# Optimization experiments

Hardware: AMD Instinct MI355X
Metric: run time of the kernel (lower is better)

## Reference

```python
import jax, jax.numpy as jnp
import numpy as np

B, N, E, H, KVC = 2, 1024, 512, 8, 1536  # KVC = 3*E, head_dim = E//H = 64
EPS = 1e-5  # torch InstanceNorm2d default eps


def instance_norm(x):
    # normalize over the last two (spatial) dims per (batch, channel); biased var, no affine
    mu = jnp.mean(x, axis=(-2, -1), keepdims=True)
    var = jnp.var(x, axis=(-2, -1), keepdims=True)
    return (x - mu) * jax.lax.rsqrt(var + EPS)


def _heads(x):
    # [B, T, E] -> [B, H, T, E//H]
    b, t, e = x.shape
    return x.reshape(b, t, H, e // H).transpose(0, 2, 1, 3)


def setup_inputs() -> dict:
    key = jax.random.key(0)
    ks = jax.random.split(key, 16)
    s_e = 1.0 / np.sqrt(E)
    s_c = 1.0 / np.sqrt(KVC)
    inp = {
        'emb1': jax.random.normal(ks[0], (B, N, E), jnp.float32),
        'emb2': jax.random.normal(ks[1], (B, N, E), jnp.float32),
        'emb3': jax.random.normal(ks[2], (B, N, E), jnp.float32),
        'emb_C': jax.random.normal(ks[3], (B, N, KVC), jnp.float32),
        'Wq1': jax.random.normal(ks[4], (E, E), jnp.float32) * s_e,
        'Wq2': jax.random.normal(ks[5], (E, E), jnp.float32) * s_e,
        'Wq3': jax.random.normal(ks[6], (E, E), jnp.float32) * s_e,
        'Wk': jax.random.normal(ks[7], (E, E), jnp.float32) * s_e,
        'Wv': jax.random.normal(ks[8], (E, E), jnp.float32) * s_e,
        'WqC': jax.random.normal(ks[9], (KVC, KVC), jnp.float32) * s_c,
        'WkC': jax.random.normal(ks[10], (KVC, KVC), jnp.float32) * s_c,
        'WvC': jax.random.normal(ks[11], (KVC, KVC), jnp.float32) * s_c,
        'Wo1': jax.random.normal(ks[12], (E, E), jnp.float32) * s_e,
        'Wo2': jax.random.normal(ks[13], (E, E), jnp.float32) * s_e,
        'Wo3': jax.random.normal(ks[14], (E, E), jnp.float32) * s_e,
    }
    return inp


def reference(emb1, emb2, emb3, emb_C, Wq1, Wq2, Wq3, Wk, Wv, WqC, WkC, WvC, Wo1, Wo2, Wo3):
    # ---- channel attention over emb_C ----
    Q_C = emb_C @ WqC.T  # [B, N, KVC]
    K_C = emb_C @ WkC.T
    V_C = emb_C @ WvC.T
    attn_c = jnp.einsum('bnc,bnd->bcd', Q_C, K_C)          # [B, KVC, KVC]
    ch_sim = jax.nn.softmax(instance_norm(attn_c), axis=-1)  # psi1 (1 channel) + softmax(dim=3)
    ctx_c = jnp.einsum('bcd,bnd->bcn', ch_sim, V_C)        # [B, KVC, N]
    T_hat = ctx_c.transpose(0, 2, 1)                        # [B, N, KVC]
    # split last dim into 3 chunks of E, concat along token dim -> shared K/V source [B, 3N, E]
    KV_S = jnp.concatenate(jnp.split(T_hat, 3, axis=2), axis=1)

    # ---- spatial attention: 3 query streams share one K/V ----
    K = _heads(KV_S @ Wk.T)                # [B, H, 3N, d]
    V = _heads(KV_S @ Wv.T)                # [B, H, 3N, d]
    Kt = K.transpose(0, 1, 3, 2)           # [B, H, d, 3N]

    def stream(emb, Wq, Wo):
        Q = _heads(emb @ Wq.T)              # [B, H, N, d]
        attn = Q @ Kt                       # [B, H, N, 3N]
        sim = jax.nn.softmax(instance_norm(attn), axis=-1)  # psi2 per (b,h) + softmax
        ctx = sim @ V                       # [B, H, N, d]
        ctx = ctx.transpose(0, 2, 1, 3).reshape(emb.shape[0], emb.shape[1], E)
        return ctx @ Wo.T

    O1 = stream(emb1, Wq1, Wo1)
    O2 = stream(emb2, Wq2, Wo2)
    O3 = stream(emb3, Wq3, Wo3)
    return (O1, O2, O3)
```

## Files before the change

### kernel.cpp

```cpp
#include <hip/hip_runtime.h>
#include <math.h>

#define NTOK 1024
#define EDIM 512
#define KVCH 1536
#define TKV  3072
#define VSTRIDE 6144

typedef __bf16 bf16x8 __attribute__((ext_vector_type(8)));
typedef float f32x4 __attribute__((ext_vector_type(4)));
#define MFMA16(a,b,c) __builtin_amdgcn_mfma_f32_16x16x32_bf16(a,b,c,0,0,0)

__device__ __forceinline__ ushort f2bf(float f){
    uint u = __float_as_uint(f);
    u += 0x7FFFu + ((u>>16)&1u);
    return (ushort)(u>>16);
}
__device__ __forceinline__ float bf2f(ushort h){ return __uint_as_float(((uint)h)<<16); }
__device__ __forceinline__ bf16x8 ldsb8(const ushort* p){ return *(const bf16x8*)p; }

__device__ __forceinline__ void async16(const ushort* g, ushort* l){
    __builtin_amdgcn_global_load_lds((const __attribute__((address_space(1))) void*)g,
                                     (__attribute__((address_space(3))) void*)l, 16, 0, 0);
}

#define NCVT 15
struct CvtJobs { const float* src[NCVT]; ushort* hi[NCVT]; ushort* lo[NCVT]; int n[NCVT]; };

__global__ __launch_bounds__(256) void cvt_hilo(CvtJobs J)
{
    int a = blockIdx.y;
    int i = (blockIdx.x*256 + threadIdx.x)*4;
    if (i >= J.n[a]) return;
    float4 v = *(const float4*)(J.src[a] + i);
    ushort4 h, l;
    h.x=f2bf(v.x); l.x=f2bf(v.x-bf2f(h.x));
    h.y=f2bf(v.y); l.y=f2bf(v.y-bf2f(h.y));
    h.z=f2bf(v.z); l.z=f2bf(v.z-bf2f(h.z));
    h.w=f2bf(v.w); l.w=f2bf(v.w-bf2f(h.w));
    *(ushort4*)(J.hi[a]+i) = h;
    *(ushort4*)(J.lo[a]+i) = l;
}

struct GemmDesc {
    const ushort *Ahi, *Alo, *Bhi, *Blo;
    float* Cf; ushort *Chi, *Clo, *Cthi, *Ctlo;
    double* stats;
    int K, lda, ldb, ldc, ldct;
    int zmod;
    long sA0, sA1, sB0, sB1, sC0, sC1;
};

__global__ __launch_bounds__(256) void mgemmF(GemmDesc D0, GemmDesc D1,
                                              int nblk0, int nx0, int ny0, int nx1, int ny1)
{
    __shared__ ushort Ah[4096], Al[4096], Bh[4096], Bl[4096];
    __shared__ double sred[8];
    const int tid = threadIdx.x;
    int bid = blockIdx.x;
    GemmDesc d; int nx, ny, rel;
    if (bid < nblk0) { d = D0; rel = bid; nx = nx0; ny = ny0; }
    else             { d = D1; rel = bid - nblk0; nx = nx1; ny = ny1; }
    const int bx = rel % nx; int tt = rel / nx;
    const int by = tt % ny;  const int z = tt / ny;
    const int zb = z / d.zmod, zj = z - zb*d.zmod;
    const size_t aoff = (size_t)zb*d.sA0 + (size_t)zj*d.sA1;
    const size_t boff = (size_t)zb*d.sB0 + (size_t)zj*d.sB1;
    const size_t coff = (size_t)zb*d.sC0 + (size_t)zj*d.sC1;
    const int mb = by<<7, nb = bx<<7;
    const int wave = tid>>6, lane = tid&63;
    const int wr = wave>>1, wc = wave&1;
    const int fr = lane&15, fq = lane>>4;
    const int srow = (wave<<5) + (lane>>2);
    const int scg  = (lane&3)<<3;
    f32x4 acc[4][4];
    #pragma unroll
    for (int i=0;i<4;++i)
        #pragma unroll
        for (int j=0;j<4;++j) acc[i][j] = (f32x4){0.f,0.f,0.f,0.f};

    for (int k0=0; k0<d.K; k0+=32) {
        #pragma unroll
        for (int it=0; it<2; ++it) {
            int row = srow + (it<<4);
            int lb = ((wave<<5) + (it<<4)) << 5;
            size_t ga = aoff + (size_t)(mb+row)*d.lda + k0 + scg;
            size_t gb = boff + (size_t)(nb+row)*d.ldb + k0 + scg;
            async16(d.Ahi+ga, &Ah[lb]);
            async16(d.Alo+ga, &Al[lb]);
            async16(d.Bhi+gb, &Bh[lb]);
            async16(d.Blo+gb, &Bl[lb]);
        }
        __syncthreads();
        bf16x8 fah[4], fal[4];
        #pragma unroll
        for (int m=0;m<4;++m) {
            int o = ((wr*64 + m*16 + fr)<<5) + (fq<<3);
            fah[m] = ldsb8(&Ah[o]); fal[m] = ldsb8(&Al[o]);
        }
        #pragma unroll
        for (int n=0;n<4;++n) {
            int o = ((wc*64 + n*16 + fr)<<5) + (fq<<3);
            bf16x8 fbh = ldsb8(&Bh[o]), fbl = ldsb8(&Bl[o]);
            #pragma unroll
            for (int m=0;m<4;++m) {
                acc[m][n] = MFMA16(fah[m], fbh, acc[m][n]);
                acc[m][n] = MFMA16(fah[m], fbl, acc[m][n]);
                acc[m][n] = MFMA16(fal[m], fbh, acc[m][n]);
            }
        }
        __syncthreads();
    }
    #pragma unroll
    for (int m=0;m<4;++m) {
        #pragma unroll
        for (int n=0;n<4;++n) {
            int row = mb + wr*64 + m*16 + fq*4;
            int col = nb + wc*64 + n*16 + fr;
            f32x4 v = acc[m][n];
            if (d.Cf) {
                #pragma unroll
                for (int r=0;r<4;++r) d.Cf[coff + (size_t)(row+r)*d.ldc + col] = v[r];
            }
            if (d.Chi) {
                #pragma unroll
                for (int r=0;r<4;++r) {
                    ushort hh = f2bf(v[r]);
                    size_t o = coff + (size_t)(row+r)*d.ldc + col;
                    d.Chi[o] = hh; d.Clo[o] = f2bf(v[r]-bf2f(hh));
                }
            }
            if (d.Cthi) {
                ushort4 h4, l4;
                #pragma unroll
                for (int r=0;r<4;++r) {
                    ushort hh = f2bf(v[r]);
                    ((ushort*)&h4)[r] = hh;
                    ((ushort*)&l4)[r] = f2bf(v[r]-bf2f(hh));
                }
                size_t o = coff + (size_t)col*d.ldct + row;
                *(ushort4*)(d.Cthi+o) = h4;
                *(ushort4*)(d.Ctlo+o) = l4;
            }
        }
    }
    if (d.stats) {
        double s=0.0, s2=0.0;
        #pragma unroll
        for (int m=0;m<4;++m)
            #pragma unroll
            for (int n=0;n<4;++n)
                #pragma unroll
                for (int r=0;r<4;++r) { double v = acc[m][n][r]; s += v; s2 += v*v; }
        #pragma unroll
        for (int off=32; off; off>>=1) { s += __shfl_xor(s, off); s2 += __shfl_xor(s2, off); }
        if (lane==0){ sred[wave]=s; sred[4+wave]=s2; }
        __syncthreads();
        if (tid==0) {
            atomicAdd(&d.stats[2*zb],   sred[0]+sred[1]+sred[2]+sred[3]);
            atomicAdd(&d.stats[2*zb+1], sred[4]+sred[5]+sred[6]+sred[7]);
        }
    }
}

__global__ __launch_bounds__(256) void chan_softmax(const float* __restrict__ ATT, const double* __restrict__ ST,
                                                    ushort* __restrict__ Shi, ushort* __restrict__ Slo)
{
    int b = blockIdx.y;
    size_t ro = (size_t)b * KVCH * KVCH + (size_t)blockIdx.x * KVCH;
    const float* p = ATT + ro;
    ushort* ph = Shi + ro;
    ushort* pl = Slo + ro;
    double cnt = (double)KVCH * (double)KVCH;
    double mean = ST[2*b] / cnt;
    double var  = ST[2*b+1] / cnt - mean * mean;
    float sc = (float)(1.0 / sqrt(var + 1e-5));
    int tid = threadIdx.x;
    float x[6];
    #pragma unroll
    for (int k = 0; k < 6; ++k) x[k] = p[tid + (k << 8)] * sc;
    float mx = fmaxf(fmaxf(fmaxf(x[0],x[1]),fmaxf(x[2],x[3])),fmaxf(x[4],x[5]));
    #pragma unroll
    for (int m = 32; m; m >>= 1) mx = fmaxf(mx, __shfl_xor(mx, m));
    __shared__ float red[4];
    int w = tid >> 6;
    if ((tid & 63) == 0) red[w] = mx;
    __syncthreads();
    mx = fmaxf(fmaxf(red[0],red[1]), fmaxf(red[2],red[3]));
    __syncthreads();
    float e[6]; float sum = 0.f;
    #pragma unroll
    for (int k = 0; k < 6; ++k) { e[k] = __expf(x[k] - mx); sum += e[k]; }
    #pragma unroll
    for (int m = 32; m; m >>= 1) sum += __shfl_xor(sum, m);
    if ((tid & 63) == 0) red[w] = sum;
    __syncthreads();
    sum = red[0]+red[1]+red[2]+red[3];
    float inv = 1.0f / sum;
    #pragma unroll
    for (int k = 0; k < 6; ++k) {
        float pv = e[k] * inv;
        ushort hh = f2bf(pv);
        ph[tid + (k << 8)] = hh;
        pl[tid + (k << 8)] = f2bf(pv - bf2f(hh));
    }
}

__global__ __launch_bounds__(256) void gram4(
    const ushort* __restrict__ Kbhi, const ushort* __restrict__ Kblo,
    const ushort* __restrict__ QBhi, const ushort* __restrict__ QBlo,
    float* __restrict__ GK, float* __restrict__ SK,
    float* __restrict__ GQ, float* __restrict__ SQm)
{
    int z = blockIdx.z;
    const ushort *Xh, *Xl; int T; float *G, *CS;
    if (z == 0) { Xh=Kbhi; Xl=Kblo; T=TKV; G=GK; CS=SK; }
    else { Xh=QBhi+(size_t)(z-1)*1048576; Xl=QBlo+(size_t)(z-1)*1048576;
           T=NTOK; G=GQ+(size_t)(z-1)*65536; CS=SQm+(size_t)(z-1)*1024; }
    int bh = blockIdx.x;
    int b = bh >> 3, h = bh & 7;
    const ushort* Xbh = Xh + (size_t)b * T * EDIM + h * 64;
    const ushort* Xbl = Xl + (size_t)b * T * EDIM + h * 64;
    int rows = T / gridDim.y;
    int t0 = blockIdx.y * rows;
    __shared__ float Xs[4][64];
    int tid = threadIdx.x;
    int i0 = (tid >> 4) << 2, j0 = (tid & 15) << 2;
    float acc[4][4] = {};
    float cs = 0.f;
    for (int t = t0; t < t0 + rows; t += 4) {
        __syncthreads();
        int r = tid >> 6, c = tid & 63;
        size_t gidx = (size_t)(t + r) * EDIM + c;
        Xs[r][c] = bf2f(Xbh[gidx]) + bf2f(Xbl[gidx]);
        __syncthreads();
        #pragma unroll
        for (int rr = 0; rr < 4; ++rr) {
            float xi0=Xs[rr][i0], xi1=Xs[rr][i0+1], xi2=Xs[rr][i0+2], xi3=Xs[rr][i0+3];
            float xj0=Xs[rr][j0], xj1=Xs[rr][j0+1], xj2=Xs[rr][j0+2], xj3=Xs[rr][j0+3];
            acc[0][0]=fmaf(xi0,xj0,acc[0][0]); acc[0][1]=fmaf(xi0,xj1,acc[0][1]); acc[0][2]=fmaf(xi0,xj2,acc[0][2]); acc[0][3]=fmaf(xi0,xj3,acc[0][3]);
            acc[1][0]=fmaf(xi1,xj0,acc[1][0]); acc[1][1]=fmaf(xi1,xj1,acc[1][1]); acc[1][2]=fmaf(xi1,xj2,acc[1][2]); acc[1][3]=fmaf(xi1,xj3,acc[1][3]);
            acc[2][0]=fmaf(xi2,xj0,acc[2][0]); acc[2][1]=fmaf(xi2,xj1,acc[2][1]); acc[2][2]=fmaf(xi2,xj2,acc[2][2]); acc[2][3]=fmaf(xi2,xj3,acc[2][3]);
            acc[3][0]=fmaf(xi3,xj0,acc[3][0]); acc[3][1]=fmaf(xi3,xj1,acc[3][1]); acc[3][2]=fmaf(xi3,xj2,acc[3][2]); acc[3][3]=fmaf(xi3,xj3,acc[3][3]);
        }
        if (tid < 64) cs += Xs[0][tid] + Xs[1][tid] + Xs[2][tid] + Xs[3][tid];
    }
    float* Gp = G + (size_t)bh * 4096;
    #pragma unroll
    for (int i = 0; i < 4; ++i)
        #pragma unroll
        for (int j = 0; j < 4; ++j)
            atomicAdd(&Gp[(i0 + i) * 64 + j0 + j], acc[i][j]);
    if (tid < 64) atomicAdd(&CS[bh * 64 + tid], cs);
}

__global__ __launch_bounds__(256) void spatial_scale(
    const float* __restrict__ GQ, const float* __restrict__ GK,
    const float* __restrict__ SQm, const float* __restrict__ SKm, float* __restrict__ SVo)
{
    int st = blockIdx.y, bh = blockIdx.x, tid = threadIdx.x;
    const float* gq = GQ + (size_t)st*65536 + bh*4096;
    const float* gk = GK + bh*4096;
    double e2 = 0.0;
    for (int i = tid; i < 4096; i += 256)
        e2 += (double)gq[i] * (double)gk[i];
    double mm = 0.0;
    if (tid < 64) mm = (double)SQm[(size_t)st*1024 + bh*64 + tid] * (double)SKm[bh*64 + tid];
    #pragma unroll
    for (int m = 32; m; m >>= 1) { e2 += __shfl_xor(e2, m); mm += __shfl_xor(mm, m); }
    __shared__ double se[4], sm[4];
    int w = tid >> 6;
    if ((tid & 63) == 0) { se[w] = e2; sm[w] = mm; }
    __syncthreads();
    if (tid == 0) {
        double cnt = (double)NTOK * (double)TKV;
        double E2 = (se[0]+se[1]+se[2]+se[3]) / cnt;
        double M  = (sm[0]+sm[1]+sm[2]+sm[3]) / cnt;
        double var = E2 - M * M;
        SVo[st*16+bh] = (float)(1.0 / sqrt(var + 1e-5));
    }
}

__global__ __launch_bounds__(256) void flash_mfma(
    const ushort* __restrict__ Qhi, const ushort* __restrict__ Qlo,
    const ushort* __restrict__ Khi, const ushort* __restrict__ Klo,
    const ushort* __restrict__ VThi, const ushort* __restrict__ VTlo,
    const float* __restrict__ SV,
    ushort* __restrict__ Ohi, ushort* __restrict__ Olo)
{
    __shared__ ushort Kh[4096], Kl[4096], Vh[4096], Vl[4096], Ph[4096];
    const int st = blockIdx.z, bh = blockIdx.y, b = bh>>3, h = bh&7;
    const int n0 = blockIdx.x<<6;
    const int tid = threadIdx.x, wave = tid>>6, lane = tid&63;
    const int fr = lane&15, fq = lane>>4;
    const float sc = SV[st*16 + bh];
    const size_t qb = (size_t)st*1048576 + (size_t)(b*1024 + n0)*512 + h*64;
    bf16x8 qfh[2], qfl[2];
    {
        const ushort* qph = Qhi + qb + (size_t)(wave*16 + fr)*512;
        const ushort* qpl = Qlo + qb + (size_t)(wave*16 + fr)*512;
        #pragma unroll
        for (int ks=0; ks<2; ++ks) {
            qfh[ks] = ldsb8(qph + ks*32 + fq*8);
            qfl[ks] = ldsb8(qpl + ks*32 + fq*8);
        }
    }
    f32x4 accO[4]; float lsum[4];
    #pragma unroll
    for (int i=0;i<4;++i){ accO[i]=(f32x4){0.f,0.f,0.f,0.f}; lsum[i]=0.f; }
    const size_t kb = (size_t)(b*TKV)*512 + h*64;
    const size_t vb = (size_t)(h*64)*VSTRIDE + b*TKV;
    for (int t0=0; t0<TKV; t0+=64) {
        #pragma unroll
        for (int it=0; it<2; ++it) {
            int r  = (wave<<4) + (it<<3) + (lane>>3);
            int lb = ((wave<<4) + (it<<3)) << 6;
            int gck = ((lane&7) ^ (r&7)) << 3;
            size_t gk = kb + (size_t)(t0+r)*512 + gck;
            size_t gv = vb + (size_t)r*VSTRIDE + t0 + gck;
            async16(Khi+gk, &Kh[lb]);
            async16(Klo+gk, &Kl[lb]);
            async16(VThi+gv, &Vh[lb]);
            async16(VTlo+gv, &Vl[lb]);
        }
        __syncthreads();
        f32x4 s[4];
        #pragma unroll
        for (int i=0;i<4;++i) s[i]=(f32x4){0.f,0.f,0.f,0.f};
        #pragma unroll
        for (int ks=0; ks<2; ++ks) {
            #pragma unroll
            for (int nf=0; nf<4; ++nf) {
                int r = nf*16+fr;
                int ko = (r<<6) + ((ks*32 + fq*8) ^ ((r&7)<<3));
                bf16x8 kh = ldsb8(&Kh[ko]), kl = ldsb8(&Kl[ko]);
                s[nf] = MFMA16(qfh[ks], kh, s[nf]);
                s[nf] = MFMA16(qfh[ks], kl, s[nf]);
                s[nf] = MFMA16(qfl[ks], kh, s[nf]);
            }
        }
        #pragma unroll
        for (int reg=0; reg<4; ++reg) {
            int prow = fq*4+reg;
            float psum = 0.f;
            #pragma unroll
            for (int nf=0;nf<4;++nf){
                float p = __expf(sc * s[nf][reg]);
                psum += p;
                int pidx = (wave<<10) + (prow<<6) + ((nf*16+fr) ^ ((prow&7)<<3));
                Ph[pidx] = f2bf(p);
            }
            lsum[reg] += psum;
        }
        #pragma unroll
        for (int ks=0; ks<2; ++ks) {
            int po = (wave<<10) + (fr<<6) + ((ks*32 + fq*8) ^ ((fr&7)<<3));
            bf16x8 ph = ldsb8(&Ph[po]);
            #pragma unroll
            for (int df=0; df<4; ++df) {
                int dd = df*16+fr;
                int vo = (dd<<6) + ((ks*32 + fq*8) ^ ((dd&7)<<3));
                bf16x8 vh = ldsb8(&Vh[vo]), vl = ldsb8(&Vl[vo]);
                accO[df] = MFMA16(ph, vh, accO[df]);
                accO[df] = MFMA16(ph, vl, accO[df]);
            }
        }
        __syncthreads();
    }
    #pragma unroll
    for (int reg=0; reg<4; ++reg) {
        #pragma unroll
        for (int m=1; m<16; m<<=1) lsum[reg] += __shfl_xor(lsum[reg], m, 16);
        float inv = 1.f/lsum[reg];
        int row = n0 + wave*16 + fq*4 + reg;
        #pragma unroll
        for (int df=0; df<4; ++df) {
            float v = accO[df][reg]*inv;
            size_t o = (size_t)st*1048576 + (size_t)(b*1024+row)*512 + h*64 + df*16 + fr;
            ushort hh = f2bf(v);
            Ohi[o] = hh; Olo[o] = f2bf(v-bf2f(hh));
        }
    }
}

constexpr size_t OFF_CH  = 0;
constexpr size_t OFF_GK  = 64;
constexpr size_t OFF_SK  = 262208;
constexpr size_t OFF_GQ  = 266304;
constexpr size_t OFF_SQM = 1052736;
constexpr size_t OFF_SV  = 1065024;
constexpr size_t ZERO_BYTES = 1065024;
constexpr size_t S0 = 1065472;
constexpr size_t S1 = S0 + 8388608;
constexpr size_t S2 = S1 + 28311552;
constexpr size_t S3 = S2 + 12582912;
constexpr size_t S4 = S3 + 12582912;
constexpr size_t S5 = S4 + 12582912;
constexpr size_t S6 = S5 + 12582912;

extern "C" void kernel_launch(void* const* d_in, const int* in_sizes, int n_in,
                              void* d_out, int out_size, void* d_ws, size_t ws_size,
                              hipStream_t stream)
{
    const float* emb[3] = {(const float*)d_in[0], (const float*)d_in[1], (const float*)d_in[2]};
    const float* embC = (const float*)d_in[3];
    const float* WqF[3] = {(const float*)d_in[4], (const float*)d_in[5], (const float*)d_in[6]};
    const float* WkF  = (const float*)d_in[7];
    const float* WvF  = (const float*)d_in[8];
    const float* WCF[3] = {(const float*)d_in[9], (const float*)d_in[10], (const float*)d_in[11]};
    const float* WoF[3] = {(const float*)d_in[12], (const float*)d_in[13], (const float*)d_in[14]};
    float* out = (float*)d_out;
    char* ws = (char*)d_ws;

    auto U16 = [&](size_t off)->ushort* { return (ushort*)(ws + off); };
    auto F32 = [&](size_t off)->float*  { return (float*)(ws + off); };

    double* CH = (double*)(ws + OFF_CH);
    float *GK = F32(OFF_GK), *SK = F32(OFF_SK), *GQ = F32(OFF_GQ), *SQm = F32(OFF_SQM), *SV = F32(OFF_SV);

    auto W8hi = [&](int i){ return U16(S0 + (size_t)i*1048576); };
    auto W8lo = [&](int i){ return U16(S0 + (size_t)i*1048576 + 524288); };
    auto WChi = [&](int i){ return U16(S1 + (size_t)i*9437184); };
    auto WClo = [&](int i){ return U16(S1 + (size_t)i*9437184 + 4718592); };
    ushort *embChi=U16(S2), *embClo=U16(S2+6291456);
    ushort *embhi=U16(S3), *emblo=U16(S3+6291456);
    ushort *QCthi=U16(S4), *QCtlo=U16(S4+6291456);
    ushort *KCthi=U16(S5), *KCtlo=U16(S5+6291456);
    ushort *VChi=U16(S6), *VClo=U16(S6+6291456);
    float  *ATT = F32(S1);
    ushort *SIMhi=U16(S4), *SIMlo=U16(S4+9437184);
    ushort *KVShi=U16(S2), *KVSlo=U16(S2+6291456);
    ushort *QBhi=U16(S1), *QBlo=U16(S1+6291456);
    ushort *Kbhi=U16(S1+12582912), *Kblo=U16(S1+12582912+6291456);
    ushort *VThi=U16(S6), *VTlo=U16(S6+6291456);
    ushort *CTXhi=U16(S5), *CTXlo=U16(S5+6291456);

    dim3 blk(256);
    (void)hipMemsetAsync(d_ws, 0, ZERO_BYTES, stream);

    CvtJobs J;
    J.src[0]=embC;   J.hi[0]=embChi; J.lo[0]=embClo; J.n[0]=2048*KVCH;
    for (int s=0;s<3;++s){ J.src[1+s]=emb[s]; J.hi[1+s]=embhi+(size_t)s*1048576; J.lo[1+s]=emblo+(size_t)s*1048576; J.n[1+s]=2*NTOK*EDIM; }
    for (int s=0;s<3;++s){ J.src[4+s]=WqF[s]; J.hi[4+s]=W8hi(s); J.lo[4+s]=W8lo(s); J.n[4+s]=EDIM*EDIM; }
    J.src[7]=WkF; J.hi[7]=W8hi(3); J.lo[7]=W8lo(3); J.n[7]=EDIM*EDIM;
    J.src[8]=WvF; J.hi[8]=W8hi(4); J.lo[8]=W8lo(4); J.n[8]=EDIM*EDIM;
    for (int s=0;s<3;++s){ J.src[9+s]=WCF[s]; J.hi[9+s]=WChi(s); J.lo[9+s]=WClo(s); J.n[9+s]=KVCH*KVCH; }
    for (int s=0;s<3;++s){ J.src[12+s]=WoF[s]; J.hi[12+s]=W8hi(5+s); J.lo[12+s]=W8lo(5+s); J.n[12+s]=EDIM*EDIM; }
    cvt_hilo<<<dim3(3072, NCVT), blk, 0, stream>>>(J);

    GemmDesc Z{}; Z.zmod = 1;

    {
        GemmDesc dq = Z;
        dq.Ahi=embChi; dq.Alo=embClo; dq.Bhi=WChi(0); dq.Blo=WClo(0);
        dq.Cthi=QCthi; dq.Ctlo=QCtlo;
        dq.K=KVCH; dq.lda=KVCH; dq.ldb=KVCH; dq.ldct=NTOK;
        dq.zmod=2; dq.sA0=0; dq.sA1=(long)NTOK*KVCH; dq.sB0=4718592; dq.sB1=0;
        dq.sC0=6291456; dq.sC1=(long)KVCH*NTOK;
        GemmDesc dv = Z;
        dv.Ahi=embChi; dv.Alo=embClo; dv.Bhi=WChi(2); dv.Blo=WClo(2);
        dv.Chi=VChi; dv.Clo=VClo;
        dv.K=KVCH; dv.lda=KVCH; dv.ldb=KVCH; dv.ldc=KVCH;
        dv.sA0=(long)NTOK*KVCH; dv.sC0=(long)NTOK*KVCH;
        mgemmF<<<dim3(576), blk, 0, stream>>>(dq, dv, 384, 12, 8, 12, 8);
    }
    {
        GemmDesc da = Z;
        da.Ahi=QCthi; da.Alo=QCtlo; da.Bhi=KCthi; da.Blo=KCtlo;
        da.Cf=ATT; da.stats=CH;
        da.K=NTOK; da.lda=NTOK; da.ldb=NTOK; da.ldc=KVCH;
        da.sA0=(long)KVCH*NTOK; da.sB0=(long)KVCH*NTOK; da.sC0=(long)KVCH*KVCH;
        mgemmF<<<dim3(288), blk, 0, stream>>>(da, da, 288, 12, 12, 1, 1);
    }
    chan_softmax<<<dim3(1536,2), blk, 0, stream>>>(ATT, CH, SIMhi, SIMlo);
    {
        GemmDesc dk = Z;
        dk.Ahi=VChi; dk.Alo=VClo; dk.Bhi=SIMhi; dk.Blo=SIMlo;
        dk.Chi=KVShi; dk.Clo=KVSlo;
        dk.K=KVCH; dk.lda=KVCH; dk.ldb=KVCH; dk.ldc=EDIM;
        dk.zmod=3; dk.sA0=(long)NTOK*KVCH; dk.sA1=0;
        dk.sB0=(long)KVCH*KVCH; dk.sB1=(long)EDIM*KVCH;
        dk.sC0=(long)TKV*EDIM; dk.sC1=(long)NTOK*EDIM;
        GemmDesc dqp = Z;
        dqp.Ahi=embhi; dqp.Alo=emblo; dqp.Bhi=W8hi(0); dqp.Blo=W8lo(0);
        dqp.Chi=QBhi; dqp.Clo=QBlo;
        dqp.K=EDIM; dqp.lda=EDIM; dqp.ldb=EDIM; dqp.ldc=EDIM;
        dqp.sA0=1048576; dqp.sB0=524288; dqp.sC0=1048576;
        mgemmF<<<dim3(384), blk, 0, stream>>>(dk, dqp, 192, 4, 8, 4, 16);
    }
    {
        GemmDesc dkp = Z;
        dkp.Ahi=KVShi; dkp.Alo=KVSlo; dkp.Bhi=W8hi(3); dkp.Blo=W8lo(3);
        dkp.Chi=Kbhi; dkp.Clo=Kblo;
        dkp.K=EDIM; dkp.lda=EDIM; dkp.ldb=EDIM; dkp.ldc=EDIM;
        GemmDesc dvp = Z;
        dvp.Ahi=KVShi; dvp.Alo=KVSlo; dvp.Bhi=W8hi(4); dvp.Blo=W8lo(4);
        dvp.Cthi=VThi; dvp.Ctlo=VTlo;
        dvp.K=EDIM; dvp.lda=EDIM; dvp.ldb=EDIM; dvp.ldct=VSTRIDE;
        mgemmF<<<dim3(384), blk, 0, stream>>>(dkp, dvp, 192, 4, 48, 4, 48);
    }
    gram4<<<dim3(16,8,4), blk, 0, stream>>>(Kbhi, Kblo, QBhi, QBlo, GK, SK, GQ, SQm);
    spatial_scale<<<dim3(16,3), blk, 0, stream>>>(GQ, GK, SQm, SK, SV);
    flash_mfma<<<dim3(16,16,3), blk, 0, stream>>>(QBhi, QBlo, Kbhi, Kblo, VThi, VTlo, SV, CTXhi, CTXlo);
    {
        GemmDesc dop = Z;
        dop.Ahi=CTXhi; dop.Alo=CTXlo; dop.Bhi=W8hi(5); dop.Blo=W8lo(5);
        dop.Cf=out;
        dop.K=EDIM; dop.lda=EDIM; dop.ldb=EDIM; dop.ldc=EDIM;
        dop.sA0=1048576; dop.sB0=524288; dop.sC0=1048576;
        mgemmF<<<dim3(192), blk, 0, stream>>>(dop, dop, 192, 4, 16, 1, 1);
    }
}
```

Baseline: 656.6 us.

## Double-buffer LDS tiles in GEMM and flash kernels with swizzled layout

Both the split-bf16 GEMM and the flash attention kernel now prefetch the next K-tile into a second LDS buffer while the current tile is consumed by MFMAs, replacing load-sync-compute with an overlapped pipeline. The GEMM also packs the hi and lo halves of each row into one 64-element LDS row with an XOR swizzle, which is meant to cut bank conflicts and merge the staging loops. This doubles the shared memory per block, which may lower occupancy, especially in the flash kernel where it grows to about 72KB. It also relies on a single barrier per iteration to order the async loads against the reads of the alternate buffer.

```diff
diff --git a/kernel.cpp b/kernel.cpp
--- a/kernel.cpp
+++ b/kernel.cpp
@@ -51,10 +51,22 @@
     long sA0, sA1, sB0, sB1, sC0, sC1;
 };
 
+__device__ __forceinline__ void stage_ab(const ushort* hi, const ushort* lo, int ld, int k0,
+                                         ushort* lds, int wave, int lane)
+{
+    #pragma unroll
+    for (int i=0;i<4;++i){
+        int r = (i<<5) + (wave<<3) + (lane>>3);
+        int g = (lane&7) ^ (r&7);
+        const ushort* s = ((g&4) ? lo : hi) + (size_t)r*ld + k0 + ((g&3)<<3);
+        async16(s, lds + (((i<<5) + (wave<<3))<<6));
+    }
+}
+
 __global__ __launch_bounds__(256) void mgemmF(GemmDesc D0, GemmDesc D1,
                                               int nblk0, int nx0, int ny0, int nx1, int ny1)
 {
-    __shared__ ushort Ah[4096], Al[4096], Bh[4096], Bl[4096];
+    __shared__ ushort A2[2][8192], B2[2][8192];
     __shared__ double sred[8];
     const int tid = threadIdx.x;
     int bid = blockIdx.x;
@@ -64,44 +76,44 @@
     const int bx = rel % nx; int tt = rel / nx;
     const int by = tt % ny;  const int z = tt / ny;
     const int zb = z / d.zmod, zj = z - zb*d.zmod;
-    const size_t aoff = (size_t)zb*d.sA0 + (size_t)zj*d.sA1;
-    const size_t boff = (size_t)zb*d.sB0 + (size_t)zj*d.sB1;
+    const int mb = by<<7, nb = bx<<7;
+    const ushort* Ah = d.Ahi + (size_t)zb*d.sA0 + (size_t)zj*d.sA1 + (size_t)mb*d.lda;
+    const ushort* Al = d.Alo + (size_t)zb*d.sA0 + (size_t)zj*d.sA1 + (size_t)mb*d.lda;
+    const ushort* Bh = d.Bhi + (size_t)zb*d.sB0 + (size_t)zj*d.sB1 + (size_t)nb*d.ldb;
+    const ushort* Bl = d.Blo + (size_t)zb*d.sB0 + (size_t)zj*d.sB1 + (size_t)nb*d.ldb;
     const size_t coff = (size_t)zb*d.sC0 + (size_t)zj*d.sC1;
-    const int mb = by<<7, nb = bx<<7;
     const int wave = tid>>6, lane = tid&63;
     const int wr = wave>>1, wc = wave&1;
     const int fr = lane&15, fq = lane>>4;
-    const int srow = (wave<<5) + (lane>>2);
-    const int scg  = (lane&3)<<3;
     f32x4 acc[4][4];
     #pragma unroll
     for (int i=0;i<4;++i)
         #pragma unroll
         for (int j=0;j<4;++j) acc[i][j] = (f32x4){0.f,0.f,0.f,0.f};
 
+    stage_ab(Ah, Al, d.lda, 0, A2[0], wave, lane);
+    stage_ab(Bh, Bl, d.ldb, 0, B2[0], wave, lane);
+    __syncthreads();
+    int cur = 0;
     for (int k0=0; k0<d.K; k0+=32) {
-        #pragma unroll
-        for (int it=0; it<2; ++it) {
-            int row = srow + (it<<4);
-            int lb = ((wave<<5) + (it<<4)) << 5;
-            size_t ga = aoff + (size_t)(mb+row)*d.lda + k0 + scg;
-            size_t gb = boff + (size_t)(nb+row)*d.ldb + k0 + scg;
-            async16(d.Ahi+ga, &Ah[lb]);
-            async16(d.Alo+ga, &Al[lb]);
-            async16(d.Bhi+gb, &Bh[lb]);
-            async16(d.Blo+gb, &Bl[lb]);
-        }
-        __syncthreads();
+        if (k0+32 < d.K) {
+            stage_ab(Ah, Al, d.lda, k0+32, A2[cur^1], wave, lane);
+            stage_ab(Bh, Bl, d.ldb, k0+32, B2[cur^1], wave, lane);
+        }
         bf16x8 fah[4], fal[4];
         #pragma unroll
         for (int m=0;m<4;++m) {
-            int o = ((wr*64 + m*16 + fr)<<5) + (fq<<3);
-            fah[m] = ldsb8(&Ah[o]); fal[m] = ldsb8(&Al[o]);
+            int r = wr*64 + m*16 + fr;
+            const ushort* base = &A2[cur][r<<6];
+            fah[m] = ldsb8(base + ((fq ^ (r&7))<<3));
+            fal[m] = ldsb8(base + (((fq|4) ^ (r&7))<<3));
         }
         #pragma unroll
         for (int n=0;n<4;++n) {
-            int o = ((wc*64 + n*16 + fr)<<5) + (fq<<3);
-            bf16x8 fbh = ldsb8(&Bh[o]), fbl = ldsb8(&Bl[o]);
+            int r = wc*64 + n*16 + fr;
+            const ushort* base = &B2[cur][r<<6];
+            bf16x8 fbh = ldsb8(base + ((fq ^ (r&7))<<3));
+            bf16x8 fbl = ldsb8(base + (((fq|4) ^ (r&7))<<3));
             #pragma unroll
             for (int m=0;m<4;++m) {
                 acc[m][n] = MFMA16(fah[m], fbh, acc[m][n]);
@@ -110,6 +122,7 @@
             }
         }
         __syncthreads();
+        cur ^= 1;
     }
     #pragma unroll
     for (int m=0;m<4;++m) {
@@ -288,7 +301,7 @@
     const float* __restrict__ SV,
     ushort* __restrict__ Ohi, ushort* __restrict__ Olo)
 {
-    __shared__ ushort Kh[4096], Kl[4096], Vh[4096], Vl[4096], Ph[4096];
+    __shared__ ushort Kh[2][4096], Kl[2][4096], Vh[2][4096], Vl[2][4096], Ph[4096];
     const int st = blockIdx.z, bh = blockIdx.y, b = bh>>3, h = bh&7;
     const int n0 = blockIdx.x<<6;
     const int tid = threadIdx.x, wave = tid>>6, lane = tid&63;
@@ -310,20 +323,27 @@
     for (int i=0;i<4;++i){ accO[i]=(f32x4){0.f,0.f,0.f,0.f}; lsum[i]=0.f; }
     const size_t kb = (size_t)(b*TKV)*512 + h*64;
     const size_t vb = (size_t)(h*64)*VSTRIDE + b*TKV;
-    for (int t0=0; t0<TKV; t0+=64) {
+
+    auto stage_kv = [&](int tn, int buf){
         #pragma unroll
         for (int it=0; it<2; ++it) {
             int r  = (wave<<4) + (it<<3) + (lane>>3);
             int lb = ((wave<<4) + (it<<3)) << 6;
             int gck = ((lane&7) ^ (r&7)) << 3;
-            size_t gk = kb + (size_t)(t0+r)*512 + gck;
-            size_t gv = vb + (size_t)r*VSTRIDE + t0 + gck;
-            async16(Khi+gk, &Kh[lb]);
-            async16(Klo+gk, &Kl[lb]);
-            async16(VThi+gv, &Vh[lb]);
-            async16(VTlo+gv, &Vl[lb]);
-        }
-        __syncthreads();
+            size_t gk = kb + (size_t)(tn+r)*512 + gck;
+            size_t gv = vb + (size_t)r*VSTRIDE + tn + gck;
+            async16(Khi+gk, &Kh[buf][lb]);
+            async16(Klo+gk, &Kl[buf][lb]);
+            async16(VThi+gv, &Vh[buf][lb]);
+            async16(VTlo+gv, &Vl[buf][lb]);
+        }
+    };
+
+    stage_kv(0, 0);
+    __syncthreads();
+    int cur = 0;
+    for (int t0=0; t0<TKV; t0+=64) {
+        if (t0+64 < TKV) stage_kv(t0+64, cur^1);
         f32x4 s[4];
         #pragma unroll
         for (int i=0;i<4;++i) s[i]=(f32x4){0.f,0.f,0.f,0.f};
@@ -333,7 +353,7 @@
             for (int nf=0; nf<4; ++nf) {
                 int r = nf*16+fr;
                 int ko = (r<<6) + ((ks*32 + fq*8) ^ ((r&7)<<3));
-                bf16x8 kh = ldsb8(&Kh[ko]), kl = ldsb8(&Kl[ko]);
+                bf16x8 kh = ldsb8(&Kh[cur][ko]), kl = ldsb8(&Kl[cur][ko]);
                 s[nf] = MFMA16(qfh[ks], kh, s[nf]);
                 s[nf] = MFMA16(qfh[ks], kl, s[nf]);
                 s[nf] = MFMA16(qfl[ks], kh, s[nf]);
@@ -360,12 +380,13 @@
             for (int df=0; df<4; ++df) {
                 int dd = df*16+fr;
                 int vo = (dd<<6) + ((ks*32 + fq*8) ^ ((dd&7)<<3));
-                bf16x8 vh = ldsb8(&Vh[vo]), vl = ldsb8(&Vl[vo]);
+                bf16x8 vh = ldsb8(&Vh[cur][vo]), vl = ldsb8(&Vl[cur][vo]);
                 accO[df] = MFMA16(ph, vh, accO[df]);
                 accO[df] = MFMA16(ph, vl, accO[df]);
             }
         }
         __syncthreads();
+        cur ^= 1;
     }
     #pragma unroll
     for (int reg=0; reg<4; ++reg) {
```

Result: slower. 684.0 us (+4.2%).
